# Kernel tuning notes

Hardware: AMD Instinct MI355X
Metric: run time of the kernel (lower is better)

Reference implementation:

```python
import jax, jax.numpy as jnp
import numpy as np

DIM = 64
HEADS = 4

def setup_inputs() -> dict:
    key = jax.random.key(0)
    ks = jax.random.split(key, 8)
    b, c, h, w = 2, DIM, 64, 64
    x = jax.random.normal(ks[0], (b, c, h, w), dtype=jnp.float32)
    illu_feat = jax.random.normal(ks[1], (b, c, h, w), dtype=jnp.float32)
    s = 0.05
    qkv_w = jax.random.normal(ks[2], (3 * c, c), dtype=jnp.float32) * s
    qkv_b = jax.random.normal(ks[3], (3 * c,), dtype=jnp.float32) * s
    illu_w = jax.random.normal(ks[4], (c, c), dtype=jnp.float32) * s
    illu_b = jax.random.normal(ks[5], (c,), dtype=jnp.float32) * s
    proj_w = jax.random.normal(ks[6], (c, c), dtype=jnp.float32) * s
    proj_b = jax.random.normal(ks[7], (c,), dtype=jnp.float32) * s
    return {"x": x, "illu_feat": illu_feat, "qkv_w": qkv_w, "qkv_b": qkv_b,
            "illu_w": illu_w, "illu_b": illu_b, "proj_w": proj_w, "proj_b": proj_b}

def reference(x, illu_feat, qkv_w, qkv_b, illu_w, illu_b, proj_w, proj_b):
    b, c, h, w = x.shape
    heads = HEADS
    d = c // heads
    scale = float(d) ** -0.5
    hw = h * w
    # 1x1 convs are per-pixel matmuls over the channel dim
    xt = x.reshape(b, c, hw).transpose(0, 2, 1)            # [b, hw, c]
    qkv = xt @ qkv_w.T + qkv_b                              # [b, hw, 3c]
    # channel layout of qkv conv output is (three, heads, d)
    qkv = qkv.reshape(b, hw, 3, heads, d).transpose(2, 0, 3, 1, 4)  # [3, b, heads, hw, d]
    q, k, v = qkv[0], qkv[1], qkv[2]
    it = illu_feat.reshape(b, c, hw).transpose(0, 2, 1) @ illu_w.T + illu_b  # [b, hw, c]
    illu = it.reshape(b, hw, heads, d).transpose(0, 2, 1, 3)                 # [b, heads, hw, d]
    k = k + illu
    attn = jax.nn.softmax(jnp.einsum('bhnd,bhmd->bhnm', q, k) * scale, axis=-1)
    out = jnp.einsum('bhnm,bhmd->bhnd', attn, v)            # [b, heads, hw, d]
    out = out.transpose(0, 2, 1, 3).reshape(b, hw, c)       # channels = (heads, d)
    y = out @ proj_w.T + proj_b                             # [b, hw, c]
    return y.transpose(0, 2, 1).reshape(b, c, h, w)
```

## Files before the change

kernel.cpp:

```cpp
#include <hip/hip_runtime.h>
#include <hip/hip_bf16.h>
#include <math.h>

#define HW   4096
#define NC   64
#define NB   2
#define NHD  4
#define DH   16
#define NBH  (NB*NHD)

typedef __attribute__((ext_vector_type(4))) float f32x4;
typedef __attribute__((ext_vector_type(8))) short bf16x8;
typedef __attribute__((ext_vector_type(2))) unsigned int uint2v;

#define QSCALE 0.36067376022224087f

static __device__ __forceinline__ unsigned short bf16_bits(float f) {
    union { __hip_bfloat16 h; unsigned short u; } cv;
    cv.h = __float2bfloat16(f);
    return cv.u;
}
static __device__ __forceinline__ float bits_to_f(unsigned short b) {
    return __uint_as_float(((unsigned int)b) << 16);
}
static __device__ __forceinline__ unsigned int cvt_pk_bf16(float lo, float hi) {
    unsigned int r;
    asm("v_cvt_pk_bf16_f32 %0, %1, %2" : "=v"(r) : "v"(lo), "v"(hi));
    return r;
}

__global__ __launch_bounds__(256) void wprep_kernel(
    const float* __restrict__ qkv_w, const float* __restrict__ qkv_b,
    const float* __restrict__ illu_w, const float* __restrict__ illu_b,
    ushort* __restrict__ Wt, float* __restrict__ Bias)
{
    int idx = blockIdx.x * 256 + threadIdx.x;
    if (idx < 49152) {
        int k8 = idx & 15;
        int n  = (idx >> 4) & 15;
        int hl = (idx >> 8) & 1;
        int ct = (idx >> 9) & 7;
        int ot = idx >> 12;
        int c   = ct*16 + k8;
        int out = ot*16 + n;
        float w;
        if (ot < 4)       w = (c < 64) ? qkv_w[out*64 + c] * QSCALE : 0.f;
        else if (ot < 8)  w = (c < 64) ? qkv_w[out*64 + c]
                                       : illu_w[(out-64)*64 + (c-64)];
        else              w = (c < 64) ? qkv_w[out*64 + c] : 0.f;
        unsigned short hb = bf16_bits(w);
        Wt[idx] = (hl == 0) ? hb : bf16_bits(w - bits_to_f(hb));
    } else if (idx < 49152 + 192) {
        int out = idx - 49152;
        float bv = (out < 64)  ? qkv_b[out] * QSCALE
                 : (out < 128) ? qkv_b[out] + illu_b[out-64]
                 :               qkv_b[out];
        Bias[out] = bv;
    }
}

__global__ __launch_bounds__(256) void qkv_kernel(
    const float* __restrict__ x, const float* __restrict__ illu,
    const ushort* __restrict__ Wt, const float* __restrict__ Bias,
    ushort* __restrict__ Qx, ushort* __restrict__ Kx, ushort* __restrict__ Vt)
{
    __shared__ alignas(16) float  xf[128*20];
    __shared__ alignas(16) ushort frag[8*16*32];

    int blk = blockIdx.x;
    int b   = blk & 1;
    int px0 = (blk >> 1) * 16;
    int tid = threadIdx.x;
    int w   = tid >> 6;
    int lane = tid & 63;
    int g   = lane >> 4;
    int n   = lane & 15;

    #pragma unroll
    for (int rep = 0; rep < 2; ++rep) {
        int id  = tid + rep*256;
        int row = id >> 2, seg = id & 3;
        const float* src = (row < 64) ? x    + (size_t)(b*NC + row)*HW
                                      : illu + (size_t)(b*NC + row - 64)*HW;
        float4 v = *(const float4*)(src + px0 + seg*4);
        *(float4*)(xf + row*20 + seg*4) = v;
    }
    __syncthreads();

    if (tid < 128) {
        int ct = tid >> 4, px = tid & 15;
        int swz = (px & 3) ^ ((px >> 2) & 3);
        union { ushort us[8]; bf16x8 v; } g0, g1, g2, g3;
        #pragma unroll
        for (int i = 0; i < 8; ++i) {
            float v  = xf[(ct*16 + i)*20 + px];
            unsigned short hb = bf16_bits(v);
            g0.us[i] = hb;
            g2.us[i] = bf16_bits(v - bits_to_f(hb));
            float v2 = xf[(ct*16 + 8 + i)*20 + px];
            unsigned short hb2 = bf16_bits(v2);
            g1.us[i] = hb2;
            g3.us[i] = bf16_bits(v2 - bits_to_f(hb2));
        }
        ushort* fb = frag + (ct*16 + px)*32;
        *(bf16x8*)(fb + ((0 ^ swz)*8)) = g0.v;
        *(bf16x8*)(fb + ((1 ^ swz)*8)) = g1.v;
        *(bf16x8*)(fb + ((2 ^ swz)*8)) = g2.v;
        *(bf16x8*)(fb + ((3 ^ swz)*8)) = g3.v;
    }
    __syncthreads();

    f32x4 zero4 = {0.f, 0.f, 0.f, 0.f};
    int px  = n;
    int swz = (px & 3) ^ ((px >> 2) & 3);
    const ushort* af_base = frag + px*32 + (g ^ swz)*8;

    #pragma unroll
    for (int j = 0; j < 3; ++j) {
        int ot  = w + 4*j;
        int nct = (ot >= 4 && ot < 8) ? 8 : 4;
        f32x4 acc = zero4;
        for (int ct = 0; ct < nct; ++ct) {
            bf16x8 af = *(const bf16x8*)(af_base + ct*512);
            const ushort* wb = Wt + ((size_t)(ot*8 + ct)*2)*256 + n*16 + (g&1)*8;
            bf16x8 bh = *(const bf16x8*)(wb);
            bf16x8 bl = *(const bf16x8*)(wb + 256);
            acc = __builtin_amdgcn_mfma_f32_16x16x32_bf16(af, bh, acc, 0, 0, 0);
            acc = __builtin_amdgcn_mfma_f32_16x16x32_bf16(af, bl, acc, 0, 0, 0);
        }
        float bias = Bias[ot*16 + n];
        float v0 = acc.x + bias, v1 = acc.y + bias;
        float v2 = acc.z + bias, v3 = acc.w + bias;
        if (ot < 8) {
            ushort* dst = (ot < 4) ? Qx : Kx;
            int head = ot & 3;
            size_t base = ((size_t)(b*NHD + head))*HW*32;
            #pragma unroll
            for (int r = 0; r < 4; ++r) {
                float val = (r==0? v0 : r==1? v1 : r==2? v2 : v3);
                int pxr = px0 + 4*g + r;
                unsigned short hb = bf16_bits(val);
                dst[base + (size_t)pxr*32 + n]      = hb;
                dst[base + (size_t)pxr*32 + 16 + n] = bf16_bits(val - bits_to_f(hb));
            }
        } else {
            int co = (ot - 8)*16 + n;
            uint2v pk;
            pk.x = cvt_pk_bf16(v0, v1);
            pk.y = cvt_pk_bf16(v2, v3);
            *(uint2v*)(Vt + ((size_t)(b*NC + co))*HW + px0 + 4*g) = pk;
        }
    }
}

#define KT   64
#define SPL  4
#define KPS  1024
#define NTS  (KPS/KT)

__global__ __launch_bounds__(512) void attn_kernel(
    const ushort* __restrict__ Qx, const ushort* __restrict__ Kx,
    const ushort* __restrict__ Vt, float* __restrict__ O)
{
    __shared__ alignas(16) ushort Ks[SPL][2][64*32];
    __shared__ alignas(16) ushort Vs[SPL][2][16*72];

    int blk  = blockIdx.x;
    int bh   = blk & 7;
    int q0   = (blk >> 3) * 64;
    int tid  = threadIdx.x;
    int w    = tid >> 6;
    int s    = w >> 1;
    int u    = w & 1;
    int lane = tid & 63;
    int g    = lane >> 4;
    int qc   = lane & 15;

    const ushort* Qb = Qx + (size_t)bh*HW*32;
    const ushort* Kb = Kx + (size_t)bh*HW*32 + (size_t)s*KPS*32;
    const ushort* Vb = Vt + (size_t)bh*DH*HW;

    int qrow0 = q0 + (u*2 + 0)*16 + qc;
    int qrow1 = q0 + (u*2 + 1)*16 + qc;
    bf16x8 qhi0 = *(const bf16x8*)(Qb + (size_t)qrow0*32 +      8*(g&1));
    bf16x8 qlo0 = *(const bf16x8*)(Qb + (size_t)qrow0*32 + 16 + 8*(g&1));
    bf16x8 qhi1 = *(const bf16x8*)(Qb + (size_t)qrow1*32 +      8*(g&1));
    bf16x8 qlo1 = *(const bf16x8*)(Qb + (size_t)qrow1*32 + 16 + 8*(g&1));

    f32x4 zero4 = {0.f, 0.f, 0.f, 0.f};
    f32x4 oacc0 = zero4, oacc1 = zero4;
    f32x4 lacc0 = zero4, lacc1 = zero4;

    int mconst = (qc & 3) ^ ((qc >> 2) & 3);
    const int koff = qc*32 + ((g ^ mconst)*8);
    const int voff = qc*72 + 4*g;

    int gt = tid & 127;
    int f0 = gt,        r0 = f0 >> 2, h0 = f0 & 3;
    int f1 = gt + 128,  r1 = f1 >> 2, h1 = f1 & 3;
    int s0 = (h0 ^ ((r0 & 3) ^ ((r0 >> 2) & 3))) * 8;
    int s1 = (h1 ^ ((r1 & 3) ^ ((r1 >> 2) & 3))) * 8;
    int vd = gt >> 3, vseg = gt & 7;

    {
        bf16x8 a0 = *(const bf16x8*)(Kb + (size_t)r0*32 + 8*h0);
        bf16x8 a1 = *(const bf16x8*)(Kb + (size_t)r1*32 + 8*h1);
        bf16x8 av = *(const bf16x8*)(Vb + (size_t)vd*HW + s*KPS + vseg*8);
        *(bf16x8*)(&Ks[s][0][0] + r0*32 + s0) = a0;
        *(bf16x8*)(&Ks[s][0][0] + r1*32 + s1) = a1;
        *(bf16x8*)(&Vs[s][0][0] + vd*72 + vseg*8) = av;
    }
    bf16x8 k0b = *(const bf16x8*)(Kb + (size_t)(KT + r0)*32 + 8*h0);
    bf16x8 k1b = *(const bf16x8*)(Kb + (size_t)(KT + r1)*32 + 8*h1);
    bf16x8 vb_ = *(const bf16x8*)(Vb + (size_t)vd*HW + s*KPS + KT + vseg*8);

    for (int t = 0; t < NTS; ++t) {
        __syncthreads();
        bf16x8 k0c = k0b, k1c = k1b, vc_ = vb_;
        if (t + 2 < NTS) {
            int kt = (t + 2) * KT;
            k0c = *(const bf16x8*)(Kb + (size_t)(kt + r0)*32 + 8*h0);
            k1c = *(const bf16x8*)(Kb + (size_t)(kt + r1)*32 + 8*h1);
            vc_ = *(const bf16x8*)(Vb + (size_t)vd*HW + s*KPS + kt + vseg*8);
        }

        const ushort* kr = &Ks[s][t & 1][0] + koff;
        const ushort* vr = &Vs[s][t & 1][0] + voff;
        unsigned int pe00 = 0, pe01 = 0, pe10 = 0, pe11 = 0;
        #pragma unroll
        for (int kb = 0; kb < 4; ++kb) {
            bf16x8 kfrag = *(const bf16x8*)(kr + kb*512);
            f32x4 sA = __builtin_amdgcn_mfma_f32_16x16x32_bf16(kfrag, qhi0, zero4, 0, 0, 0);
            sA = __builtin_amdgcn_mfma_f32_16x16x32_bf16(kfrag, qlo0, sA, 0, 0, 0);
            float a0 = __builtin_amdgcn_exp2f(sA.x);
            float a1 = __builtin_amdgcn_exp2f(sA.y);
            float a2 = __builtin_amdgcn_exp2f(sA.z);
            float a3 = __builtin_amdgcn_exp2f(sA.w);
            lacc0.x += a0; lacc0.y += a1; lacc0.z += a2; lacc0.w += a3;
            unsigned int alo = cvt_pk_bf16(a0, a1);
            unsigned int ahi = cvt_pk_bf16(a2, a3);
            f32x4 sB = __builtin_amdgcn_mfma_f32_16x16x32_bf16(kfrag, qhi1, zero4, 0, 0, 0);
            sB = __builtin_amdgcn_mfma_f32_16x16x32_bf16(kfrag, qlo1, sB, 0, 0, 0);
            float b0 = __builtin_amdgcn_exp2f(sB.x);
            float b1 = __builtin_amdgcn_exp2f(sB.y);
            float b2 = __builtin_amdgcn_exp2f(sB.z);
            float b3 = __builtin_amdgcn_exp2f(sB.w);
            lacc1.x += b0; lacc1.y += b1; lacc1.z += b2; lacc1.w += b3;
            unsigned int blo = cvt_pk_bf16(b0, b1);
            unsigned int bhi = cvt_pk_bf16(b2, b3);

            if ((kb & 1) == 0) { pe00 = alo; pe01 = ahi; pe10 = blo; pe11 = bhi; }
            else {
                uint2v vE = *(const uint2v*)(vr + (kb-1)*16);
                uint2v vO = *(const uint2v*)(vr + kb*16);
                union { unsigned int uu[4]; bf16x8 h; } pa, vv;
                vv.uu[0] = vE.x; vv.uu[1] = vE.y; vv.uu[2] = vO.x; vv.uu[3] = vO.y;
                pa.uu[0] = pe00; pa.uu[1] = pe01; pa.uu[2] = alo; pa.uu[3] = ahi;
                oacc0 = __builtin_amdgcn_mfma_f32_16x16x32_bf16(pa.h, vv.h, oacc0, 0, 0, 0);
                pa.uu[0] = pe10; pa.uu[1] = pe11; pa.uu[2] = blo; pa.uu[3] = bhi;
                oacc1 = __builtin_amdgcn_mfma_f32_16x16x32_bf16(pa.h, vv.h, oacc1, 0, 0, 0);
            }
        }

        if (t + 1 < NTS) {
            int nb = (t + 1) & 1;
            *(bf16x8*)(&Ks[s][nb][0] + r0*32 + s0) = k0b;
            *(bf16x8*)(&Ks[s][nb][0] + r1*32 + s1) = k1b;
            *(bf16x8*)(&Vs[s][nb][0] + vd*72 + vseg*8) = vb_;
            k0b = k0c; k1b = k1c; vb_ = vc_;
        }
    }

    float l0 = (lacc0.x + lacc0.y) + (lacc0.z + lacc0.w);
    l0 += __shfl_xor(l0, 16);
    l0 += __shfl_xor(l0, 32);
    float l1 = (lacc1.x + lacc1.y) + (lacc1.z + lacc1.w);
    l1 += __shfl_xor(l1, 16);
    l1 += __shfl_xor(l1, 32);

    __syncthreads();
    float* mrgF = (float*)&Ks[0][0][0];
    if (s > 0) {
        float* m0 = mrgF + (((((s-1)*2 + u)*2 + 0)*64 + lane)*5);
        m0[0] = oacc0.x; m0[1] = oacc0.y; m0[2] = oacc0.z; m0[3] = oacc0.w; m0[4] = l0;
        float* m1 = mrgF + (((((s-1)*2 + u)*2 + 1)*64 + lane)*5);
        m1[0] = oacc1.x; m1[1] = oacc1.y; m1[2] = oacc1.z; m1[3] = oacc1.w; m1[4] = l1;
    }
    __syncthreads();
    if (s == 0) {
        #pragma unroll
        for (int sp = 0; sp < 3; ++sp) {
            const float* m0 = mrgF + ((((sp*2 + u)*2 + 0)*64 + lane)*5);
            oacc0.x += m0[0]; oacc0.y += m0[1]; oacc0.z += m0[2]; oacc0.w += m0[3];
            l0 += m0[4];
            const float* m1 = mrgF + ((((sp*2 + u)*2 + 1)*64 + lane)*5);
            oacc1.x += m1[0]; oacc1.y += m1[1]; oacc1.z += m1[2]; oacc1.w += m1[3];
            l1 += m1[4];
        }
        int b = bh >> 2, h = bh & 3;
        float* Ob0 = O + ((size_t)b*HW + q0 + (u*2 + 0)*16)*NC + h*DH;
        float* Ob1 = O + ((size_t)b*HW + q0 + (u*2 + 1)*16)*NC + h*DH;
        #pragma unroll
        for (int r = 0; r < 4; ++r) {
            float lr0 = __shfl(l0, 4*g + r);
            float ov0 = (r==0? oacc0.x : r==1? oacc0.y : r==2? oacc0.z : oacc0.w);
            Ob0[(4*g + r)*NC + qc] = ov0 / lr0;
            float lr1 = __shfl(l1, 4*g + r);
            float ov1 = (r==0? oacc1.x : r==1? oacc1.y : r==2? oacc1.z : oacc1.w);
            Ob1[(4*g + r)*NC + qc] = ov1 / lr1;
        }
    }
}

__global__ __launch_bounds__(256) void proj_kernel(
    const float* __restrict__ O, const float* __restrict__ proj_w,
    const float* __restrict__ proj_b, float* __restrict__ y)
{
    const int PIX = 8;
    __shared__ float os[PIX][NC];
    __shared__ float ys[NC][PIX+1];
    int blk = blockIdx.x;
    int b   = blk >> 9;
    int p0  = (blk & 511) * PIX;
    int tid = threadIdx.x;
    int c   = tid & 63;
    int pg  = tid >> 6;

    if (tid < PIX*NC/4) {
        int pp = tid >> 4, c4 = tid & 15;
        ((float4*)os[pp])[c4] = ((const float4*)(O + ((size_t)(b*HW + p0 + pp))*NC))[c4];
    }
    float wv[NC];
    #pragma unroll
    for (int c4 = 0; c4 < NC/4; c4++) {
        float4 t = ((const float4*)(proj_w + (size_t)c*NC))[c4];
        wv[4*c4+0] = t.x; wv[4*c4+1] = t.y; wv[4*c4+2] = t.z; wv[4*c4+3] = t.w;
    }
    float bias = proj_b[c];
    __syncthreads();

    #pragma unroll
    for (int u = 0; u < 2; ++u) {
        int pi = pg*2 + u;
        float a0 = 0.f, a1 = 0.f, a2 = 0.f, a3 = 0.f;
        #pragma unroll
        for (int c4 = 0; c4 < NC/4; c4++) {
            float4 ov = ((const float4*)os[pi])[c4];
            a0 = fmaf(wv[4*c4+0], ov.x, a0);
            a1 = fmaf(wv[4*c4+1], ov.y, a1);
            a2 = fmaf(wv[4*c4+2], ov.z, a2);
            a3 = fmaf(wv[4*c4+3], ov.w, a3);
        }
        ys[c][pi] = bias + ((a0 + a1) + (a2 + a3));
    }
    __syncthreads();
    for (int idx = tid; idx < PIX*NC; idx += 256) {
        int cc = idx >> 3;
        int i  = idx & 7;
        y[(size_t)(b*NC + cc)*HW + p0 + i] = ys[cc][i];
    }
}

extern "C" void kernel_launch(void* const* d_in, const int* in_sizes, int n_in,
                              void* d_out, int out_size, void* d_ws, size_t ws_size,
                              hipStream_t stream)
{
    const float* x      = (const float*)d_in[0];
    const float* illu   = (const float*)d_in[1];
    const float* qkv_w  = (const float*)d_in[2];
    const float* qkv_b  = (const float*)d_in[3];
    const float* illu_w = (const float*)d_in[4];
    const float* illu_b = (const float*)d_in[5];
    const float* proj_w = (const float*)d_in[6];
    const float* proj_b = (const float*)d_in[7];
    float* out = (float*)d_out;

    ushort* Qx   = (ushort*)d_ws;
    ushort* Kx   = Qx + (size_t)NBH*HW*32;
    ushort* Vt   = Kx + (size_t)NBH*HW*32;
    float*  O    = (float*)(Vt + (size_t)NBH*HW*DH);
    ushort* Wt   = (ushort*)(O + (size_t)NB*HW*NC);
    float*  Bias = (float*)(Wt + 49152);

    hipLaunchKernelGGL(wprep_kernel, dim3(193), dim3(256), 0, stream,
                       qkv_w, qkv_b, illu_w, illu_b, Wt, Bias);
    hipLaunchKernelGGL(qkv_kernel, dim3(512), dim3(256), 0, stream,
                       x, illu, Wt, Bias, Qx, Kx, Vt);
    hipLaunchKernelGGL(attn_kernel, dim3(512), dim3(512), 0, stream,
                       Qx, Kx, Vt, O);
    hipLaunchKernelGGL(proj_kernel, dim3(1024), dim3(256), 0, stream,
                       O, proj_w, proj_b, out);
}
```

Measured before the change: 54.92 us.

## Move output projection onto bf16 MFMA with split hi/lo weights and activations

The proj kernel now uses bf16 MFMA 16x16x32 in place of scalar FP32 FMAs. Weights are pre-split into hi/lo bf16 pairs in wprep, and O tiles are converted into swizzled hi/lo fragments in shared memory. Each block handles 16 pixels and all 64 output channels, and writes float4 stores through an LDS transpose. This removes the per-thread 64-float weight register load and the scalar FMA work. In exchange it adds conversion overhead and an approximated precision scheme.

```diff
diff --git a/kernel.cpp b/kernel.cpp
--- a/kernel.cpp
+++ b/kernel.cpp
@@ -32,7 +32,8 @@
 __global__ __launch_bounds__(256) void wprep_kernel(
     const float* __restrict__ qkv_w, const float* __restrict__ qkv_b,
     const float* __restrict__ illu_w, const float* __restrict__ illu_b,
-    ushort* __restrict__ Wt, float* __restrict__ Bias)
+    const float* __restrict__ proj_w,
+    ushort* __restrict__ Wt, float* __restrict__ Bias, ushort* __restrict__ Wp)
 {
     int idx = blockIdx.x * 256 + threadIdx.x;
     if (idx < 49152) {
@@ -50,12 +51,22 @@
         else              w = (c < 64) ? qkv_w[out*64 + c] : 0.f;
         unsigned short hb = bf16_bits(w);
         Wt[idx] = (hl == 0) ? hb : bf16_bits(w - bits_to_f(hb));
-    } else if (idx < 49152 + 192) {
+    } else if (idx < 49344) {
         int out = idx - 49152;
         float bv = (out < 64)  ? qkv_b[out] * QSCALE
                  : (out < 128) ? qkv_b[out] + illu_b[out-64]
                  :               qkv_b[out];
         Bias[out] = bv;
+    } else if (idx < 49344 + 8192) {
+        int local = idx - 49344;
+        int k8 = local & 15;
+        int n  = (local >> 4) & 15;
+        int hl = (local >> 8) & 1;
+        int ct = (local >> 9) & 3;
+        int ot = local >> 11;
+        float w = proj_w[(ot*16 + n)*64 + ct*16 + k8];
+        unsigned short hb = bf16_bits(w);
+        Wp[local] = (hl == 0) ? hb : bf16_bits(w - bits_to_f(hb));
     }
 }
 
@@ -313,51 +324,81 @@
 }
 
 __global__ __launch_bounds__(256) void proj_kernel(
-    const float* __restrict__ O, const float* __restrict__ proj_w,
+    const float* __restrict__ O, const ushort* __restrict__ Wp,
     const float* __restrict__ proj_b, float* __restrict__ y)
 {
-    const int PIX = 8;
-    __shared__ float os[PIX][NC];
-    __shared__ float ys[NC][PIX+1];
+    __shared__ alignas(16) float  of[64*20];
+    __shared__ alignas(16) ushort frag[4*16*32];
+    __shared__ alignas(16) float  ys[64][20];
+
     int blk = blockIdx.x;
-    int b   = blk >> 9;
-    int p0  = (blk & 511) * PIX;
+    int b   = blk & 1;
+    int px0 = (blk >> 1) * 16;
     int tid = threadIdx.x;
-    int c   = tid & 63;
-    int pg  = tid >> 6;
-
-    if (tid < PIX*NC/4) {
-        int pp = tid >> 4, c4 = tid & 15;
-        ((float4*)os[pp])[c4] = ((const float4*)(O + ((size_t)(b*HW + p0 + pp))*NC))[c4];
-    }
-    float wv[NC];
+    int w   = tid >> 6;
+    int lane = tid & 63;
+    int g   = lane >> 4;
+    int n   = lane & 15;
+
+    {
+        int px = tid >> 4, c4 = tid & 15;
+        float4 v = *(const float4*)(O + ((size_t)(b*HW + px0 + px))*NC + c4*4);
+        of[(c4*4+0)*20 + px] = v.x;
+        of[(c4*4+1)*20 + px] = v.y;
+        of[(c4*4+2)*20 + px] = v.z;
+        of[(c4*4+3)*20 + px] = v.w;
+    }
+    __syncthreads();
+
+    if (tid < 64) {
+        int ct = tid >> 4, px = tid & 15;
+        int swz = (px & 3) ^ ((px >> 2) & 3);
+        union { ushort us[8]; bf16x8 v; } g0, g1, g2, g3;
+        #pragma unroll
+        for (int i = 0; i < 8; ++i) {
+            float v  = of[(ct*16 + i)*20 + px];
+            unsigned short hb = bf16_bits(v);
+            g0.us[i] = hb;
+            g2.us[i] = bf16_bits(v - bits_to_f(hb));
+            float v2 = of[(ct*16 + 8 + i)*20 + px];
+            unsigned short hb2 = bf16_bits(v2);
+            g1.us[i] = hb2;
+            g3.us[i] = bf16_bits(v2 - bits_to_f(hb2));
+        }
+        ushort* fb = frag + (ct*16 + px)*32;
+        *(bf16x8*)(fb + ((0 ^ swz)*8)) = g0.v;
+        *(bf16x8*)(fb + ((1 ^ swz)*8)) = g1.v;
+        *(bf16x8*)(fb + ((2 ^ swz)*8)) = g2.v;
+        *(bf16x8*)(fb + ((3 ^ swz)*8)) = g3.v;
+    }
+    __syncthreads();
+
+    f32x4 acc = {0.f, 0.f, 0.f, 0.f};
+    int px  = n;
+    int swz = (px & 3) ^ ((px >> 2) & 3);
+    const ushort* af_base = frag + px*32 + (g ^ swz)*8;
     #pragma unroll
-    for (int c4 = 0; c4 < NC/4; c4++) {
-        float4 t = ((const float4*)(proj_w + (size_t)c*NC))[c4];
-        wv[4*c4+0] = t.x; wv[4*c4+1] = t.y; wv[4*c4+2] = t.z; wv[4*c4+3] = t.w;
-    }
-    float bias = proj_b[c];
-    __syncthreads();
-
-    #pragma unroll
-    for (int u = 0; u < 2; ++u) {
-        int pi = pg*2 + u;
-        float a0 = 0.f, a1 = 0.f, a2 = 0.f, a3 = 0.f;
-        #pragma unroll
-        for (int c4 = 0; c4 < NC/4; c4++) {
-            float4 ov = ((const float4*)os[pi])[c4];
-            a0 = fmaf(wv[4*c4+0], ov.x, a0);
-            a1 = fmaf(wv[4*c4+1], ov.y, a1);
-            a2 = fmaf(wv[4*c4+2], ov.z, a2);
-            a3 = fmaf(wv[4*c4+3], ov.w, a3);
-        }
-        ys[c][pi] = bias + ((a0 + a1) + (a2 + a3));
-    }
-    __syncthreads();
-    for (int idx = tid; idx < PIX*NC; idx += 256) {
-        int cc = idx >> 3;
-        int i  = idx & 7;
-        y[(size_t)(b*NC + cc)*HW + p0 + i] = ys[cc][i];
+    for (int ct = 0; ct < 4; ++ct) {
+        bf16x8 af = *(const bf16x8*)(af_base + ct*512);
+        const ushort* wb = Wp + ((size_t)(w*4 + ct)*2)*256 + n*16 + (g&1)*8;
+        bf16x8 bh = *(const bf16x8*)(wb);
+        bf16x8 bl = *(const bf16x8*)(wb + 256);
+        acc = __builtin_amdgcn_mfma_f32_16x16x32_bf16(af, bh, acc, 0, 0, 0);
+        acc = __builtin_amdgcn_mfma_f32_16x16x32_bf16(af, bl, acc, 0, 0, 0);
+    }
+    float bias = proj_b[w*16 + n];
+    ys[w*16 + n][4*g+0] = acc.x + bias;
+    ys[w*16 + n][4*g+1] = acc.y + bias;
+    ys[w*16 + n][4*g+2] = acc.z + bias;
+    ys[w*16 + n][4*g+3] = acc.w + bias;
+    __syncthreads();
+
+    {
+        int row = tid >> 2, seg = tid & 3;
+        float4 v;
+        v.x = ys[row][seg*4+0]; v.y = ys[row][seg*4+1];
+        v.z = ys[row][seg*4+2]; v.w = ys[row][seg*4+3];
+        *(float4*)(y + ((size_t)(b*NC + row))*HW + px0 + seg*4) = v;
     }
 }
 
@@ -381,13 +422,14 @@
     float*  O    = (float*)(Vt + (size_t)NBH*HW*DH);
     ushort* Wt   = (ushort*)(O + (size_t)NB*HW*NC);
     float*  Bias = (float*)(Wt + 49152);
-
-    hipLaunchKernelGGL(wprep_kernel, dim3(193), dim3(256), 0, stream,
-                       qkv_w, qkv_b, illu_w, illu_b, Wt, Bias);
+    ushort* Wp   = (ushort*)(Bias + 192);
+
+    hipLaunchKernelGGL(wprep_kernel, dim3(225), dim3(256), 0, stream,
+                       qkv_w, qkv_b, illu_w, illu_b, proj_w, Wt, Bias, Wp);
     hipLaunchKernelGGL(qkv_kernel, dim3(512), dim3(256), 0, stream,
                        x, illu, Wt, Bias, Qx, Kx, Vt);
     hipLaunchKernelGGL(attn_kernel, dim3(512), dim3(512), 0, stream,
                        Qx, Kx, Vt, O);
-    hipLaunchKernelGGL(proj_kernel, dim3(1024), dim3(256), 0, stream,
-                       O, proj_w, proj_b, out);
-}
+    hipLaunchKernelGGL(proj_kernel, dim3(512), dim3(256), 0, stream,
+                       O, Wp, proj_b, out);
+}
```

New measurement: 48.18 us. -12.3%, faster.
